# Kernel optimization log

Measured on AMD Instinct MI355X. Metric: run time of the kernel, lower is better.

The kernel has to match this reference:

```python
import jax, jax.numpy as jnp
import numpy as np

B, N, D, H = 4, 2048, 512, 8
HEAD = D // H
TEMP = 8.0


def setup_inputs() -> dict:
    key = jax.random.key(0)
    k1, k2, k3, k4 = jax.random.split(key, 4)
    return {
        "keys": jax.random.normal(k1, (B, N, D), dtype=jnp.float32),
        "queries": jax.random.normal(k2, (B, N, D), dtype=jnp.float32),
        "values": jax.random.normal(k3, (B, N, D), dtype=jnp.float32),
        "W_comb": jax.random.normal(k4, (D, D), dtype=jnp.float32) * (1.0 / np.sqrt(D)),
        "b_comb": jnp.zeros((D,), dtype=jnp.float32),
    }


def reference(keys, queries, values, W_comb, b_comb):
    b, nk, d = keys.shape
    nq = queries.shape[1]
    h, hd = H, HEAD
    # split heads: (b, n, d) -> (b, n, h, hd)
    k = keys.reshape(b, nk, h, hd)
    q = queries.reshape(b, nq, h, hd)
    v = values.reshape(b, nk, h, hd)
    # scaled dot-product attention per head
    logits = jnp.einsum("bqhd,bkhd->bhqk", q, k) / TEMP  # (b, h, nq, nk)
    w = jax.nn.softmax(logits, axis=-1)
    out = jnp.einsum("bhqk,bkhd->bqhd", w, v).reshape(b, nq, d)
    # head_combine: Linear with bias (torch: x @ W.T + b)
    return out @ W_comb.T + b_comb
```

## Files before the change

### kernel.cpp

```cpp
#include <hip/hip_runtime.h>

#define B_ 4
#define N_ 2048
#define D_ 512
#define H_ 8

typedef __attribute__((ext_vector_type(8))) short bf16x8;
typedef __attribute__((ext_vector_type(4))) short bf16x4;
typedef __attribute__((ext_vector_type(4))) float f32x4;

__device__ __forceinline__ unsigned short f32_to_bf16(float f) {
  unsigned int u = __float_as_uint(f);
  u += 0x7FFFu + ((u >> 16) & 1u);
  return (unsigned short)(u >> 16);
}

__device__ __forceinline__ unsigned int pack2_bf16(float a, float b) {
#if __has_builtin(__builtin_amdgcn_cvt_pk_bf16_f32)
  typedef __attribute__((ext_vector_type(2))) __bf16 bf16v2;
  bf16v2 r = __builtin_amdgcn_cvt_pk_bf16_f32(a, b);
  return *(unsigned int*)&r;
#else
  return (unsigned int)f32_to_bf16(a) | ((unsigned int)f32_to_bf16(b) << 16);
#endif
}

__device__ __forceinline__ float fast_exp2(float x) {
#if __has_builtin(__builtin_amdgcn_exp2f)
  return __builtin_amdgcn_exp2f(x);
#else
  return exp2f(x);
#endif
}

__device__ __forceinline__ f32x4 mfma16(bf16x4 a, bf16x4 b, f32x4 c) {
#if __has_builtin(__builtin_amdgcn_mfma_f32_16x16x16_bf16)
  return __builtin_amdgcn_mfma_f32_16x16x16_bf16(a, b, c, 0, 0, 0);
#else
  return __builtin_amdgcn_mfma_f32_16x16x16bf16_1k(a, b, c, 0, 0, 0);
#endif
}

__global__ __launch_bounds__(256) void convert_kernel(
    const float* __restrict__ Kf, const float* __restrict__ Qf,
    const float* __restrict__ Vf, const float* __restrict__ Wf,
    unsigned short* __restrict__ Qb, unsigned short* __restrict__ Kb,
    unsigned short* __restrict__ Wb, unsigned short* __restrict__ Vt) {
  __shared__ float tile[64 * 72];
  const int tid = threadIdx.x;
  if (blockIdx.x < 1024) {
    const float qs = 0.125f * 1.4426950408889634f;
    int gid = blockIdx.x * 256 + tid;
    const float4* Q4 = (const float4*)Qf;
    const float4* K4 = (const float4*)Kf;
    for (int i = gid; i < (B_ * N_ * D_) / 4; i += 262144) {
      float4 q = Q4[i];
      ((uint2*)Qb)[i] = make_uint2(pack2_bf16(q.x * qs, q.y * qs),
                                   pack2_bf16(q.z * qs, q.w * qs));
      float4 k = K4[i];
      ((uint2*)Kb)[i] = make_uint2(pack2_bf16(k.x, k.y), pack2_bf16(k.z, k.w));
    }
    if (gid < (D_ * D_) / 4) {
      float4 w = ((const float4*)Wf)[gid];
      ((uint2*)Wb)[gid] = make_uint2(pack2_bf16(w.x, w.y), pack2_bf16(w.z, w.w));
    }
  } else {
    int bid = blockIdx.x - 1024;
    int nt = bid & 31, bh = bid >> 5;
    int b = bh >> 3, h = bh & 7;
    int n0 = nt * 64;
#pragma unroll
    for (int i = 0; i < 4; ++i) {
      int idx = i * 256 + tid;
      int r = idx >> 4, c = idx & 15;
      *(float4*)&tile[r * 72 + c * 4] =
          *(const float4*)(Vf + (size_t)(b * N_ + n0 + r) * D_ + h * 64 + c * 4);
    }
    __syncthreads();
    int d = tid >> 2, c = tid & 3;
    unsigned int o[8];
#pragma unroll
    for (int j = 0; j < 8; ++j)
      o[j] = pack2_bf16(tile[(c * 16 + 2 * j) * 72 + d],
                        tile[(c * 16 + 2 * j + 1) * 72 + d]);
    unsigned short* dst = Vt + ((size_t)bh * 64 + d) * N_ + n0 + c * 16;
    *(bf16x8*)dst = *(bf16x8*)&o[0];
    *(bf16x8*)(dst + 8) = *(bf16x8*)&o[4];
  }
}

__global__ __launch_bounds__(256, 4) void attn_kernel(
    const unsigned short* __restrict__ Qb, const unsigned short* __restrict__ Kb,
    const unsigned short* __restrict__ Vt, unsigned short* __restrict__ Ob) {
  __shared__ unsigned short Kl[2][64 * 72];
  __shared__ unsigned short Vl[2][64 * 72];

  const int tid = threadIdx.x;
  const int w = tid >> 6;
  const int lane = tid & 63;
  const int lr = lane & 15;
  const int lq = lane >> 4;

  const int bh = blockIdx.y;
  const int qb = blockIdx.x * 64;
  const size_t slab = (size_t)(bh >> 3) * N_ * D_ + (size_t)(bh & 7) * 64;
  const unsigned short* kbase = Kb + slab;
  const unsigned short* vtbase = Vt + (size_t)bh * 64 * N_;

  bf16x8 qa0, qa1;
  {
    const unsigned short* qrow = Qb + slab + (size_t)(qb + w * 16 + lr) * D_;
    qa0 = *(const bf16x8*)(qrow + 8 * lq);
    qa1 = *(const bf16x8*)(qrow + 32 + 8 * lq);
  }

  f32x4 O[4];
#pragma unroll
  for (int i = 0; i < 4; ++i) O[i] = (f32x4){0.f, 0.f, 0.f, 0.f};
  float l_i = 0.f;

  const int k_dc = (tid & 7) * 8;
  const int k_r0 = tid >> 3;

  {
    const unsigned short* ksrc = kbase + (size_t)k_r0 * D_ + k_dc;
    bf16x8 a = *(const bf16x8*)ksrc;
    bf16x8 b = *(const bf16x8*)(ksrc + (size_t)32 * D_);
    const unsigned short* vsrc = vtbase + (size_t)k_r0 * N_ + k_dc;
    bf16x8 c = *(const bf16x8*)vsrc;
    bf16x8 d = *(const bf16x8*)(vsrc + (size_t)32 * N_);
    *(bf16x8*)&Kl[0][k_r0 * 72 + k_dc] = a;
    *(bf16x8*)&Kl[0][(k_r0 + 32) * 72 + k_dc] = b;
    *(bf16x8*)&Vl[0][k_r0 * 72 + k_dc] = c;
    *(bf16x8*)&Vl[0][(k_r0 + 32) * 72 + k_dc] = d;
  }

  for (int kt = 0; kt < 32; ++kt) {
    const int p = kt & 1;
    __syncthreads();

    bf16x8 nk0, nk1, nv0, nv1;
    const bool more = (kt + 1) < 32;
    if (more) {
      const int kb1 = (kt + 1) * 64;
      const unsigned short* ksrc = kbase + (size_t)(kb1 + k_r0) * D_ + k_dc;
      nk0 = *(const bf16x8*)ksrc;
      nk1 = *(const bf16x8*)(ksrc + (size_t)32 * D_);
      const unsigned short* vsrc = vtbase + (size_t)k_r0 * N_ + kb1 + k_dc;
      nv0 = *(const bf16x8*)vsrc;
      nv1 = *(const bf16x8*)(vsrc + (size_t)32 * N_);
    }

    f32x4 S[4];
#pragma unroll
    for (int nt = 0; nt < 4; ++nt) {
      bf16x8 kf0 = *(const bf16x8*)&Kl[p][(nt * 16 + lr) * 72 + 8 * lq];
      bf16x8 kf1 = *(const bf16x8*)&Kl[p][(nt * 16 + lr) * 72 + 32 + 8 * lq];
      S[nt] = __builtin_amdgcn_mfma_f32_16x16x32_bf16(
          kf0, qa0, (f32x4){0.f, 0.f, 0.f, 0.f}, 0, 0, 0);
      S[nt] = __builtin_amdgcn_mfma_f32_16x16x32_bf16(kf1, qa1, S[nt], 0, 0, 0);
    }

    bf16x4 pf[4];
#pragma unroll
    for (int nt = 0; nt < 4; ++nt) {
      float p0 = fast_exp2(S[nt][0]);
      float p1 = fast_exp2(S[nt][1]);
      float p2 = fast_exp2(S[nt][2]);
      float p3 = fast_exp2(S[nt][3]);
      l_i += (p0 + p1) + (p2 + p3);
      unsigned int lo = pack2_bf16(p0, p1);
      unsigned int hi = pack2_bf16(p2, p3);
      uint2 packed = make_uint2(lo, hi);
      pf[nt] = *(bf16x4*)&packed;
    }

#pragma unroll
    for (int dt = 0; dt < 4; ++dt) {
#pragma unroll
      for (int nt = 0; nt < 4; ++nt) {
        bf16x4 vf = *(const bf16x4*)&Vl[p][(dt * 16 + lr) * 72 + nt * 16 + 4 * lq];
        O[dt] = mfma16(vf, pf[nt], O[dt]);
      }
    }

    if (more) {
      *(bf16x8*)&Kl[1 - p][k_r0 * 72 + k_dc] = nk0;
      *(bf16x8*)&Kl[1 - p][(k_r0 + 32) * 72 + k_dc] = nk1;
      *(bf16x8*)&Vl[1 - p][k_r0 * 72 + k_dc] = nv0;
      *(bf16x8*)&Vl[1 - p][(k_r0 + 32) * 72 + k_dc] = nv1;
    }
  }

  float l = l_i;
  l += __shfl_xor(l, 16);
  l += __shfl_xor(l, 32);
  float linv = 1.0f / l;
#pragma unroll
  for (int dt = 0; dt < 4; ++dt) {
#pragma unroll
    for (int r = 0; r < 4; ++r)
      Kl[0][(w * 16 + lr) * 72 + dt * 16 + lq * 4 + r] =
          f32_to_bf16(O[dt][r] * linv);
  }
  __syncthreads();
  {
    unsigned short* dst = Ob + slab + (size_t)(qb + k_r0) * D_ + k_dc;
    *(bf16x8*)dst = *(const bf16x8*)&Kl[0][k_r0 * 72 + k_dc];
    *(bf16x8*)(dst + (size_t)32 * D_) =
        *(const bf16x8*)&Kl[0][(k_r0 + 32) * 72 + k_dc];
  }
}

__global__ __launch_bounds__(256) void gemm_kernel(
    const unsigned short* __restrict__ A, const unsigned short* __restrict__ Wb,
    const float* __restrict__ bias, float* __restrict__ out) {
  __shared__ unsigned short A_lds[2][64 * 72];
  __shared__ unsigned short W_lds[2][64 * 72];

  const int tid = threadIdx.x;
  const int w = tid >> 6;
  const int lane = tid & 63;
  const int lr = lane & 15;
  const int lq = lane >> 4;

  const int cb = blockIdx.x * 64;
  const int mb = blockIdx.y * 64;

  const int dc = (tid & 7) * 8;
  const int r0 = tid >> 3;

  f32x4 acc[4];
#pragma unroll
  for (int i = 0; i < 4; ++i) acc[i] = (f32x4){0.f, 0.f, 0.f, 0.f};

  {
    *(bf16x8*)&A_lds[0][r0 * 72 + dc] =
        *(const bf16x8*)(A + (size_t)(mb + r0) * D_ + dc);
    *(bf16x8*)&A_lds[0][(r0 + 32) * 72 + dc] =
        *(const bf16x8*)(A + (size_t)(mb + r0 + 32) * D_ + dc);
    *(bf16x8*)&W_lds[0][r0 * 72 + dc] =
        *(const bf16x8*)(Wb + (size_t)(cb + r0) * D_ + dc);
    *(bf16x8*)&W_lds[0][(r0 + 32) * 72 + dc] =
        *(const bf16x8*)(Wb + (size_t)(cb + r0 + 32) * D_ + dc);
  }

  for (int kt = 0; kt < 8; ++kt) {
    const int p = kt & 1;
    __syncthreads();

    bf16x8 na0, na1, nw0, nw1;
    const bool more = (kt + 1) < 8;
    if (more) {
      const int k1 = (kt + 1) * 64;
      na0 = *(const bf16x8*)(A + (size_t)(mb + r0) * D_ + k1 + dc);
      na1 = *(const bf16x8*)(A + (size_t)(mb + r0 + 32) * D_ + k1 + dc);
      nw0 = *(const bf16x8*)(Wb + (size_t)(cb + r0) * D_ + k1 + dc);
      nw1 = *(const bf16x8*)(Wb + (size_t)(cb + r0 + 32) * D_ + k1 + dc);
    }

    bf16x8 a0 = *(const bf16x8*)&A_lds[p][(w * 16 + lr) * 72 + 8 * lq];
    bf16x8 a1 = *(const bf16x8*)&A_lds[p][(w * 16 + lr) * 72 + 32 + 8 * lq];
#pragma unroll
    for (int nt = 0; nt < 4; ++nt) {
      bf16x8 b0 = *(const bf16x8*)&W_lds[p][(nt * 16 + lr) * 72 + 8 * lq];
      bf16x8 b1 = *(const bf16x8*)&W_lds[p][(nt * 16 + lr) * 72 + 32 + 8 * lq];
      acc[nt] = __builtin_amdgcn_mfma_f32_16x16x32_bf16(a0, b0, acc[nt], 0, 0, 0);
      acc[nt] = __builtin_amdgcn_mfma_f32_16x16x32_bf16(a1, b1, acc[nt], 0, 0, 0);
    }

    if (more) {
      *(bf16x8*)&A_lds[1 - p][r0 * 72 + dc] = na0;
      *(bf16x8*)&A_lds[1 - p][(r0 + 32) * 72 + dc] = na1;
      *(bf16x8*)&W_lds[1 - p][r0 * 72 + dc] = nw0;
      *(bf16x8*)&W_lds[1 - p][(r0 + 32) * 72 + dc] = nw1;
    }
  }

#pragma unroll
  for (int nt = 0; nt < 4; ++nt) {
    float bc = bias[cb + nt * 16 + lr];
#pragma unroll
    for (int rr = 0; rr < 4; ++rr) {
      int row = mb + w * 16 + lq * 4 + rr;
      out[(size_t)row * D_ + cb + nt * 16 + lr] = acc[nt][rr] + bc;
    }
  }
}

extern "C" void kernel_launch(void* const* d_in, const int* in_sizes, int n_in,
                              void* d_out, int out_size, void* d_ws,
                              size_t ws_size, hipStream_t stream) {
  (void)in_sizes; (void)n_in; (void)out_size; (void)ws_size;
  const float* keys    = (const float*)d_in[0];
  const float* queries = (const float*)d_in[1];
  const float* values  = (const float*)d_in[2];
  const float* W       = (const float*)d_in[3];
  const float* bias    = (const float*)d_in[4];
  float* out = (float*)d_out;

  char* ws = (char*)d_ws;
  unsigned short* Qb = (unsigned short*)(ws);
  unsigned short* Kb = (unsigned short*)(ws + 8388608);
  unsigned short* Vt = (unsigned short*)(ws + 16777216);
  unsigned short* Wb = (unsigned short*)(ws + 25165824);
  unsigned short* Ab = (unsigned short*)(ws + 25690112);

  convert_kernel<<<2048, 256, 0, stream>>>(keys, queries, values, W,
                                           Qb, Kb, Wb, Vt);

  attn_kernel<<<dim3(N_ / 64, B_ * H_), 256, 0, stream>>>(Qb, Kb, Vt, Ab);

  gemm_kernel<<<dim3(D_ / 64, (B_ * N_) / 64), 256, 0, stream>>>(Ab, Wb, bias,
                                                                 out);
}
```

Before: 175.9 us.

## Split attention keys across waves with LDS reduction and swizzled K/V tiles

Each wave now owns 16 keys of each 64-key tile and processes all 64 queries, instead of owning 16 queries over all keys. Each wave therefore loads its K and V fragments from LDS once per tile rather than four times, and the K/V tiles use an XOR-swizzled layout with no padding to avoid bank conflicts. Partial outputs and row sums are combined across the four waves through a tree reduction in a union LDS buffer at the end. In exchange, accumulator registers grow fourfold (64 floats of O per lane), the launch bound drops to 2 blocks per CU, and the epilogue adds several barriers.

Result: slower. 185.9 us (+5.7%).

```diff
diff --git a/kernel.cpp b/kernel.cpp
--- a/kernel.cpp
+++ b/kernel.cpp
@@ -39,6 +39,10 @@
 #else
   return __builtin_amdgcn_mfma_f32_16x16x16bf16_1k(a, b, c, 0, 0, 0);
 #endif
+}
+
+__device__ __forceinline__ int lds_sw(int row, int chunk) {
+  return row * 64 + ((chunk ^ (row & 7)) * 8);
 }
 
 __global__ __launch_bounds__(256) void convert_kernel(
@@ -89,11 +93,15 @@
   }
 }
 
-__global__ __launch_bounds__(256, 4) void attn_kernel(
+union AttnLDS {
+  struct { unsigned short K[2][64 * 64]; unsigned short V[2][64 * 64]; } loop;
+  struct { float O[2][64 * 68]; float l[2][64]; } red;
+};
+
+__global__ __launch_bounds__(256, 2) void attn_kernel(
     const unsigned short* __restrict__ Qb, const unsigned short* __restrict__ Kb,
     const unsigned short* __restrict__ Vt, unsigned short* __restrict__ Ob) {
-  __shared__ unsigned short Kl[2][64 * 72];
-  __shared__ unsigned short Vl[2][64 * 72];
+  __shared__ AttnLDS lds;
 
   const int tid = threadIdx.x;
   const int w = tid >> 6;
@@ -107,32 +115,35 @@
   const unsigned short* kbase = Kb + slab;
   const unsigned short* vtbase = Vt + (size_t)bh * 64 * N_;
 
-  bf16x8 qa0, qa1;
+  bf16x8 qa[4][2];
+#pragma unroll
+  for (int qt = 0; qt < 4; ++qt) {
+    const unsigned short* qrow = Qb + slab + (size_t)(qb + qt * 16 + lr) * D_;
+    qa[qt][0] = *(const bf16x8*)(qrow + 8 * lq);
+    qa[qt][1] = *(const bf16x8*)(qrow + 32 + 8 * lq);
+  }
+
+  f32x4 O[4][4];
+#pragma unroll
+  for (int i = 0; i < 4; ++i)
+#pragma unroll
+    for (int j = 0; j < 4; ++j) O[i][j] = (f32x4){0.f, 0.f, 0.f, 0.f};
+  float l_part[4] = {0.f, 0.f, 0.f, 0.f};
+
+  const int st_r = tid >> 3;
+  const int st_c = tid & 7;
+
   {
-    const unsigned short* qrow = Qb + slab + (size_t)(qb + w * 16 + lr) * D_;
-    qa0 = *(const bf16x8*)(qrow + 8 * lq);
-    qa1 = *(const bf16x8*)(qrow + 32 + 8 * lq);
-  }
-
-  f32x4 O[4];
-#pragma unroll
-  for (int i = 0; i < 4; ++i) O[i] = (f32x4){0.f, 0.f, 0.f, 0.f};
-  float l_i = 0.f;
-
-  const int k_dc = (tid & 7) * 8;
-  const int k_r0 = tid >> 3;
-
-  {
-    const unsigned short* ksrc = kbase + (size_t)k_r0 * D_ + k_dc;
+    const unsigned short* ksrc = kbase + (size_t)st_r * D_ + st_c * 8;
     bf16x8 a = *(const bf16x8*)ksrc;
     bf16x8 b = *(const bf16x8*)(ksrc + (size_t)32 * D_);
-    const unsigned short* vsrc = vtbase + (size_t)k_r0 * N_ + k_dc;
+    const unsigned short* vsrc = vtbase + (size_t)st_r * N_ + st_c * 8;
     bf16x8 c = *(const bf16x8*)vsrc;
     bf16x8 d = *(const bf16x8*)(vsrc + (size_t)32 * N_);
-    *(bf16x8*)&Kl[0][k_r0 * 72 + k_dc] = a;
-    *(bf16x8*)&Kl[0][(k_r0 + 32) * 72 + k_dc] = b;
-    *(bf16x8*)&Vl[0][k_r0 * 72 + k_dc] = c;
-    *(bf16x8*)&Vl[0][(k_r0 + 32) * 72 + k_dc] = d;
+    *(bf16x8*)&lds.loop.K[0][lds_sw(st_r, st_c)] = a;
+    *(bf16x8*)&lds.loop.K[0][lds_sw(st_r + 32, st_c)] = b;
+    *(bf16x8*)&lds.loop.V[0][lds_sw(st_r, st_c)] = c;
+    *(bf16x8*)&lds.loop.V[0][lds_sw(st_r + 32, st_c)] = d;
   }
 
   for (int kt = 0; kt < 32; ++kt) {
@@ -143,72 +154,144 @@
     const bool more = (kt + 1) < 32;
     if (more) {
       const int kb1 = (kt + 1) * 64;
-      const unsigned short* ksrc = kbase + (size_t)(kb1 + k_r0) * D_ + k_dc;
+      const unsigned short* ksrc = kbase + (size_t)(kb1 + st_r) * D_ + st_c * 8;
       nk0 = *(const bf16x8*)ksrc;
       nk1 = *(const bf16x8*)(ksrc + (size_t)32 * D_);
-      const unsigned short* vsrc = vtbase + (size_t)k_r0 * N_ + kb1 + k_dc;
+      const unsigned short* vsrc = vtbase + (size_t)st_r * N_ + kb1 + st_c * 8;
       nv0 = *(const bf16x8*)vsrc;
       nv1 = *(const bf16x8*)(vsrc + (size_t)32 * N_);
     }
 
+    bf16x8 kf0 = *(const bf16x8*)&lds.loop.K[p][lds_sw(w * 16 + lr, lq)];
+    bf16x8 kf1 = *(const bf16x8*)&lds.loop.K[p][lds_sw(w * 16 + lr, lq + 4)];
+
     f32x4 S[4];
 #pragma unroll
-    for (int nt = 0; nt < 4; ++nt) {
-      bf16x8 kf0 = *(const bf16x8*)&Kl[p][(nt * 16 + lr) * 72 + 8 * lq];
-      bf16x8 kf1 = *(const bf16x8*)&Kl[p][(nt * 16 + lr) * 72 + 32 + 8 * lq];
-      S[nt] = __builtin_amdgcn_mfma_f32_16x16x32_bf16(
-          kf0, qa0, (f32x4){0.f, 0.f, 0.f, 0.f}, 0, 0, 0);
-      S[nt] = __builtin_amdgcn_mfma_f32_16x16x32_bf16(kf1, qa1, S[nt], 0, 0, 0);
+    for (int qt = 0; qt < 4; ++qt) {
+      S[qt] = __builtin_amdgcn_mfma_f32_16x16x32_bf16(
+          kf0, qa[qt][0], (f32x4){0.f, 0.f, 0.f, 0.f}, 0, 0, 0);
+      S[qt] = __builtin_amdgcn_mfma_f32_16x16x32_bf16(kf1, qa[qt][1], S[qt],
+                                                      0, 0, 0);
     }
 
     bf16x4 pf[4];
 #pragma unroll
-    for (int nt = 0; nt < 4; ++nt) {
-      float p0 = fast_exp2(S[nt][0]);
-      float p1 = fast_exp2(S[nt][1]);
-      float p2 = fast_exp2(S[nt][2]);
-      float p3 = fast_exp2(S[nt][3]);
-      l_i += (p0 + p1) + (p2 + p3);
-      unsigned int lo = pack2_bf16(p0, p1);
-      unsigned int hi = pack2_bf16(p2, p3);
-      uint2 packed = make_uint2(lo, hi);
-      pf[nt] = *(bf16x4*)&packed;
+    for (int qt = 0; qt < 4; ++qt) {
+      float p0 = fast_exp2(S[qt][0]);
+      float p1 = fast_exp2(S[qt][1]);
+      float p2 = fast_exp2(S[qt][2]);
+      float p3 = fast_exp2(S[qt][3]);
+      l_part[qt] += (p0 + p1) + (p2 + p3);
+      uint2 packed = make_uint2(pack2_bf16(p0, p1), pack2_bf16(p2, p3));
+      pf[qt] = *(bf16x4*)&packed;
     }
 
 #pragma unroll
     for (int dt = 0; dt < 4; ++dt) {
-#pragma unroll
-      for (int nt = 0; nt < 4; ++nt) {
-        bf16x4 vf = *(const bf16x4*)&Vl[p][(dt * 16 + lr) * 72 + nt * 16 + 4 * lq];
-        O[dt] = mfma16(vf, pf[nt], O[dt]);
+      const int row = dt * 16 + lr;
+      const int scol = w * 16 + 4 * lq;
+      const int chunk = scol >> 3;
+      const int off = scol & 7;
+      bf16x4 vf = *(const bf16x4*)&lds.loop.V[p][lds_sw(row, chunk) + off];
+#pragma unroll
+      for (int qt = 0; qt < 4; ++qt)
+        O[dt][qt] = mfma16(vf, pf[qt], O[dt][qt]);
+    }
+
+    if (more) {
+      *(bf16x8*)&lds.loop.K[1 - p][lds_sw(st_r, st_c)] = nk0;
+      *(bf16x8*)&lds.loop.K[1 - p][lds_sw(st_r + 32, st_c)] = nk1;
+      *(bf16x8*)&lds.loop.V[1 - p][lds_sw(st_r, st_c)] = nv0;
+      *(bf16x8*)&lds.loop.V[1 - p][lds_sw(st_r + 32, st_c)] = nv1;
+    }
+  }
+
+#pragma unroll
+  for (int qt = 0; qt < 4; ++qt) {
+    l_part[qt] += __shfl_xor(l_part[qt], 16);
+    l_part[qt] += __shfl_xor(l_part[qt], 32);
+  }
+
+  __syncthreads();
+
+  if (w >= 2) {
+    const int g = w - 2;
+#pragma unroll
+    for (int dt = 0; dt < 4; ++dt)
+#pragma unroll
+      for (int qt = 0; qt < 4; ++qt)
+        *(f32x4*)&lds.red.O[g][(qt * 16 + lr) * 68 + dt * 16 + lq * 4] =
+            O[dt][qt];
+    if (lq == 0) {
+#pragma unroll
+      for (int qt = 0; qt < 4; ++qt)
+        lds.red.l[g][qt * 16 + lr] = l_part[qt];
+    }
+  }
+  __syncthreads();
+
+  if (w < 2) {
+    const int g = w;
+#pragma unroll
+    for (int dt = 0; dt < 4; ++dt)
+#pragma unroll
+      for (int qt = 0; qt < 4; ++qt) {
+        f32x4 t = *(const f32x4*)&lds.red
+                      .O[g][(qt * 16 + lr) * 68 + dt * 16 + lq * 4];
+        O[dt][qt][0] += t[0]; O[dt][qt][1] += t[1];
+        O[dt][qt][2] += t[2]; O[dt][qt][3] += t[3];
       }
-    }
-
-    if (more) {
-      *(bf16x8*)&Kl[1 - p][k_r0 * 72 + k_dc] = nk0;
-      *(bf16x8*)&Kl[1 - p][(k_r0 + 32) * 72 + k_dc] = nk1;
-      *(bf16x8*)&Vl[1 - p][k_r0 * 72 + k_dc] = nv0;
-      *(bf16x8*)&Vl[1 - p][(k_r0 + 32) * 72 + k_dc] = nv1;
-    }
-  }
-
-  float l = l_i;
-  l += __shfl_xor(l, 16);
-  l += __shfl_xor(l, 32);
-  float linv = 1.0f / l;
-#pragma unroll
-  for (int dt = 0; dt < 4; ++dt) {
-#pragma unroll
-    for (int r = 0; r < 4; ++r)
-      Kl[0][(w * 16 + lr) * 72 + dt * 16 + lq * 4 + r] =
-          f32_to_bf16(O[dt][r] * linv);
-  }
-  __syncthreads();
+#pragma unroll
+    for (int qt = 0; qt < 4; ++qt)
+      l_part[qt] += lds.red.l[g][qt * 16 + lr];
+  }
+  __syncthreads();
+
+  if (w == 1) {
+#pragma unroll
+    for (int dt = 0; dt < 4; ++dt)
+#pragma unroll
+      for (int qt = 0; qt < 4; ++qt)
+        *(f32x4*)&lds.red.O[0][(qt * 16 + lr) * 68 + dt * 16 + lq * 4] =
+            O[dt][qt];
+    if (lq == 0) {
+#pragma unroll
+      for (int qt = 0; qt < 4; ++qt)
+        lds.red.l[0][qt * 16 + lr] = l_part[qt];
+    }
+  }
+  __syncthreads();
+
+  unsigned short* S16 = (unsigned short*)&lds.red.O[1][0];
+  if (w == 0) {
+    float linv[4];
+#pragma unroll
+    for (int qt = 0; qt < 4; ++qt) {
+      float lt = l_part[qt] + lds.red.l[0][qt * 16 + lr];
+      linv[qt] = 1.0f / lt;
+    }
+#pragma unroll
+    for (int dt = 0; dt < 4; ++dt)
+#pragma unroll
+      for (int qt = 0; qt < 4; ++qt) {
+        f32x4 t = *(const f32x4*)&lds.red
+                      .O[0][(qt * 16 + lr) * 68 + dt * 16 + lq * 4];
+        float v0 = (O[dt][qt][0] + t[0]) * linv[qt];
+        float v1 = (O[dt][qt][1] + t[1]) * linv[qt];
+        float v2 = (O[dt][qt][2] + t[2]) * linv[qt];
+        float v3 = (O[dt][qt][3] + t[3]) * linv[qt];
+        uint2 packed = make_uint2(pack2_bf16(v0, v1), pack2_bf16(v2, v3));
+        *(bf16x4*)&S16[(qt * 16 + lr) * 72 + dt * 16 + lq * 4] =
+            *(bf16x4*)&packed;
+      }
+  }
+  __syncthreads();
+
   {
-    unsigned short* dst = Ob + slab + (size_t)(qb + k_r0) * D_ + k_dc;
-    *(bf16x8*)dst = *(const bf16x8*)&Kl[0][k_r0 * 72 + k_dc];
-    *(bf16x8*)(dst + (size_t)32 * D_) =
-        *(const bf16x8*)&Kl[0][(k_r0 + 32) * 72 + k_dc];
+    const int row = tid >> 2, ch = tid & 3;
+    unsigned short* dst = Ob + slab + (size_t)(qb + row) * D_ + ch * 16;
+    *(bf16x8*)dst = *(const bf16x8*)&S16[row * 72 + ch * 16];
+    *(bf16x8*)(dst + 8) = *(const bf16x8*)&S16[row * 72 + ch * 16 + 8];
   }
 }
 
```

## Process 128 queries per attention block to reuse K/V tiles across two row groups

Applied to the files above, without the earlier changes.

Each warp now handles two 16-row query groups, so every block covers 128 queries instead of 64. Each K/V tile staged in LDS feeds twice as many MFMAs, which halves global K/V traffic and staging work per query. The cost is more registers (launch bounds drop to 2 blocks per SM), half as many blocks (512), and lower occupancy. The output write is reworked to cover the larger 128-row tile.

Result: faster. 166.0 us (-5.6%).

```diff
diff --git a/kernel.cpp b/kernel.cpp
--- a/kernel.cpp
+++ b/kernel.cpp
@@ -89,7 +89,7 @@
   }
 }
 
-__global__ __launch_bounds__(256, 4) void attn_kernel(
+__global__ __launch_bounds__(256, 2) void attn_kernel(
     const unsigned short* __restrict__ Qb, const unsigned short* __restrict__ Kb,
     const unsigned short* __restrict__ Vt, unsigned short* __restrict__ Ob) {
   __shared__ unsigned short Kl[2][64 * 72];
@@ -102,37 +102,41 @@
   const int lq = lane >> 4;
 
   const int bh = blockIdx.y;
-  const int qb = blockIdx.x * 64;
+  const int qb = blockIdx.x * 128;
   const size_t slab = (size_t)(bh >> 3) * N_ * D_ + (size_t)(bh & 7) * 64;
   const unsigned short* kbase = Kb + slab;
   const unsigned short* vtbase = Vt + (size_t)bh * 64 * N_;
 
-  bf16x8 qa0, qa1;
+  bf16x8 qa[2][2];
+#pragma unroll
+  for (int g = 0; g < 2; ++g) {
+    const unsigned short* qrow =
+        Qb + slab + (size_t)(qb + w * 32 + g * 16 + lr) * D_;
+    qa[g][0] = *(const bf16x8*)(qrow + 8 * lq);
+    qa[g][1] = *(const bf16x8*)(qrow + 32 + 8 * lq);
+  }
+
+  f32x4 O[4][2];
+#pragma unroll
+  for (int i = 0; i < 4; ++i)
+#pragma unroll
+    for (int g = 0; g < 2; ++g) O[i][g] = (f32x4){0.f, 0.f, 0.f, 0.f};
+  float l_g[2] = {0.f, 0.f};
+
+  const int st_r = tid >> 3;
+  const int st_c = tid & 7;
+
   {
-    const unsigned short* qrow = Qb + slab + (size_t)(qb + w * 16 + lr) * D_;
-    qa0 = *(const bf16x8*)(qrow + 8 * lq);
-    qa1 = *(const bf16x8*)(qrow + 32 + 8 * lq);
-  }
-
-  f32x4 O[4];
-#pragma unroll
-  for (int i = 0; i < 4; ++i) O[i] = (f32x4){0.f, 0.f, 0.f, 0.f};
-  float l_i = 0.f;
-
-  const int k_dc = (tid & 7) * 8;
-  const int k_r0 = tid >> 3;
-
-  {
-    const unsigned short* ksrc = kbase + (size_t)k_r0 * D_ + k_dc;
+    const unsigned short* ksrc = kbase + (size_t)st_r * D_ + st_c * 8;
     bf16x8 a = *(const bf16x8*)ksrc;
     bf16x8 b = *(const bf16x8*)(ksrc + (size_t)32 * D_);
-    const unsigned short* vsrc = vtbase + (size_t)k_r0 * N_ + k_dc;
+    const unsigned short* vsrc = vtbase + (size_t)st_r * N_ + st_c * 8;
     bf16x8 c = *(const bf16x8*)vsrc;
     bf16x8 d = *(const bf16x8*)(vsrc + (size_t)32 * N_);
-    *(bf16x8*)&Kl[0][k_r0 * 72 + k_dc] = a;
-    *(bf16x8*)&Kl[0][(k_r0 + 32) * 72 + k_dc] = b;
-    *(bf16x8*)&Vl[0][k_r0 * 72 + k_dc] = c;
-    *(bf16x8*)&Vl[0][(k_r0 + 32) * 72 + k_dc] = d;
+    *(bf16x8*)&Kl[0][st_r * 72 + st_c * 8] = a;
+    *(bf16x8*)&Kl[0][(st_r + 32) * 72 + st_c * 8] = b;
+    *(bf16x8*)&Vl[0][st_r * 72 + st_c * 8] = c;
+    *(bf16x8*)&Vl[0][(st_r + 32) * 72 + st_c * 8] = d;
   }
 
   for (int kt = 0; kt < 32; ++kt) {
@@ -143,72 +147,93 @@
     const bool more = (kt + 1) < 32;
     if (more) {
       const int kb1 = (kt + 1) * 64;
-      const unsigned short* ksrc = kbase + (size_t)(kb1 + k_r0) * D_ + k_dc;
+      const unsigned short* ksrc = kbase + (size_t)(kb1 + st_r) * D_ + st_c * 8;
       nk0 = *(const bf16x8*)ksrc;
       nk1 = *(const bf16x8*)(ksrc + (size_t)32 * D_);
-      const unsigned short* vsrc = vtbase + (size_t)k_r0 * N_ + kb1 + k_dc;
+      const unsigned short* vsrc = vtbase + (size_t)st_r * N_ + kb1 + st_c * 8;
       nv0 = *(const bf16x8*)vsrc;
       nv1 = *(const bf16x8*)(vsrc + (size_t)32 * N_);
     }
 
-    f32x4 S[4];
+    f32x4 S[4][2];
 #pragma unroll
     for (int nt = 0; nt < 4; ++nt) {
       bf16x8 kf0 = *(const bf16x8*)&Kl[p][(nt * 16 + lr) * 72 + 8 * lq];
       bf16x8 kf1 = *(const bf16x8*)&Kl[p][(nt * 16 + lr) * 72 + 32 + 8 * lq];
-      S[nt] = __builtin_amdgcn_mfma_f32_16x16x32_bf16(
-          kf0, qa0, (f32x4){0.f, 0.f, 0.f, 0.f}, 0, 0, 0);
-      S[nt] = __builtin_amdgcn_mfma_f32_16x16x32_bf16(kf1, qa1, S[nt], 0, 0, 0);
-    }
-
-    bf16x4 pf[4];
-#pragma unroll
-    for (int nt = 0; nt < 4; ++nt) {
-      float p0 = fast_exp2(S[nt][0]);
-      float p1 = fast_exp2(S[nt][1]);
-      float p2 = fast_exp2(S[nt][2]);
-      float p3 = fast_exp2(S[nt][3]);
-      l_i += (p0 + p1) + (p2 + p3);
-      unsigned int lo = pack2_bf16(p0, p1);
-      unsigned int hi = pack2_bf16(p2, p3);
-      uint2 packed = make_uint2(lo, hi);
-      pf[nt] = *(bf16x4*)&packed;
-    }
+#pragma unroll
+      for (int g = 0; g < 2; ++g) {
+        S[nt][g] = __builtin_amdgcn_mfma_f32_16x16x32_bf16(
+            kf0, qa[g][0], (f32x4){0.f, 0.f, 0.f, 0.f}, 0, 0, 0);
+        S[nt][g] = __builtin_amdgcn_mfma_f32_16x16x32_bf16(kf1, qa[g][1],
+                                                           S[nt][g], 0, 0, 0);
+      }
+    }
+
+    bf16x4 pf[4][2];
+#pragma unroll
+    for (int nt = 0; nt < 4; ++nt)
+#pragma unroll
+      for (int g = 0; g < 2; ++g) {
+        float p0 = fast_exp2(S[nt][g][0]);
+        float p1 = fast_exp2(S[nt][g][1]);
+        float p2 = fast_exp2(S[nt][g][2]);
+        float p3 = fast_exp2(S[nt][g][3]);
+        l_g[g] += (p0 + p1) + (p2 + p3);
+        uint2 packed = make_uint2(pack2_bf16(p0, p1), pack2_bf16(p2, p3));
+        pf[nt][g] = *(bf16x4*)&packed;
+      }
 
 #pragma unroll
     for (int dt = 0; dt < 4; ++dt) {
 #pragma unroll
       for (int nt = 0; nt < 4; ++nt) {
-        bf16x4 vf = *(const bf16x4*)&Vl[p][(dt * 16 + lr) * 72 + nt * 16 + 4 * lq];
-        O[dt] = mfma16(vf, pf[nt], O[dt]);
+        bf16x4 vf =
+            *(const bf16x4*)&Vl[p][(dt * 16 + lr) * 72 + nt * 16 + 4 * lq];
+#pragma unroll
+        for (int g = 0; g < 2; ++g)
+          O[dt][g] = mfma16(vf, pf[nt][g], O[dt][g]);
       }
     }
 
     if (more) {
-      *(bf16x8*)&Kl[1 - p][k_r0 * 72 + k_dc] = nk0;
-      *(bf16x8*)&Kl[1 - p][(k_r0 + 32) * 72 + k_dc] = nk1;
-      *(bf16x8*)&Vl[1 - p][k_r0 * 72 + k_dc] = nv0;
-      *(bf16x8*)&Vl[1 - p][(k_r0 + 32) * 72 + k_dc] = nv1;
-    }
-  }
-
-  float l = l_i;
-  l += __shfl_xor(l, 16);
-  l += __shfl_xor(l, 32);
-  float linv = 1.0f / l;
-#pragma unroll
-  for (int dt = 0; dt < 4; ++dt) {
-#pragma unroll
-    for (int r = 0; r < 4; ++r)
-      Kl[0][(w * 16 + lr) * 72 + dt * 16 + lq * 4 + r] =
-          f32_to_bf16(O[dt][r] * linv);
+      *(bf16x8*)&Kl[1 - p][st_r * 72 + st_c * 8] = nk0;
+      *(bf16x8*)&Kl[1 - p][(st_r + 32) * 72 + st_c * 8] = nk1;
+      *(bf16x8*)&Vl[1 - p][st_r * 72 + st_c * 8] = nv0;
+      *(bf16x8*)&Vl[1 - p][(st_r + 32) * 72 + st_c * 8] = nv1;
+    }
+  }
+
+#pragma unroll
+  for (int g = 0; g < 2; ++g) {
+    l_g[g] += __shfl_xor(l_g[g], 16);
+    l_g[g] += __shfl_xor(l_g[g], 32);
+  }
+
+  __syncthreads();
+  unsigned short* SR = &Kl[0][0];
+#pragma unroll
+  for (int g = 0; g < 2; ++g) {
+    float linv = 1.0f / l_g[g];
+#pragma unroll
+    for (int dt = 0; dt < 4; ++dt) {
+      float v0 = O[dt][g][0] * linv;
+      float v1 = O[dt][g][1] * linv;
+      float v2 = O[dt][g][2] * linv;
+      float v3 = O[dt][g][3] * linv;
+      uint2 packed = make_uint2(pack2_bf16(v0, v1), pack2_bf16(v2, v3));
+      *(bf16x4*)&SR[(w * 32 + g * 16 + lr) * 72 + dt * 16 + lq * 4] =
+          *(bf16x4*)&packed;
+    }
   }
   __syncthreads();
   {
-    unsigned short* dst = Ob + slab + (size_t)(qb + k_r0) * D_ + k_dc;
-    *(bf16x8*)dst = *(const bf16x8*)&Kl[0][k_r0 * 72 + k_dc];
-    *(bf16x8*)(dst + (size_t)32 * D_) =
-        *(const bf16x8*)&Kl[0][(k_r0 + 32) * 72 + k_dc];
+    const int row = tid >> 1, half = tid & 1;
+    unsigned short* dst = Ob + slab + (size_t)(qb + row) * D_ + half * 32;
+    const unsigned short* src = &SR[row * 72 + half * 32];
+    *(bf16x8*)dst = *(const bf16x8*)src;
+    *(bf16x8*)(dst + 8) = *(const bf16x8*)(src + 8);
+    *(bf16x8*)(dst + 16) = *(const bf16x8*)(src + 16);
+    *(bf16x8*)(dst + 24) = *(const bf16x8*)(src + 24);
   }
 }
 
@@ -309,7 +334,7 @@
   convert_kernel<<<2048, 256, 0, stream>>>(keys, queries, values, W,
                                            Qb, Kb, Wb, Vt);
 
-  attn_kernel<<<dim3(N_ / 64, B_ * H_), 256, 0, stream>>>(Qb, Kb, Vt, Ab);
+  attn_kernel<<<dim3(N_ / 128, B_ * H_), 256, 0, stream>>>(Qb, Kb, Vt, Ab);
 
   gemm_kernel<<<dim3(D_ / 64, (B_ * N_) / 64), 256, 0, stream>>>(Ab, Wb, bias,
                                                                  out);
```
